# Kernel tuning notes

Hardware: AMD Instinct MI355X
Metric: run time of the kernel (lower is better)

Reference implementation:

```python
import jax, jax.numpy as jnp
from jax import lax
import numpy as np

# torch.sign(torch.sign(x) + 0.5): maps x<0 -> -1, x>=0 -> +1 (zeros go to +1)
def binarize(x):
    return jnp.where(x >= 0, 1.0, -1.0).astype(x.dtype)


def setup_inputs() -> dict:
    key = jax.random.key(0)
    kx, kw, kb = jax.random.split(key, 3)
    x = jax.random.normal(kx, (32, 256, 56, 56), dtype=jnp.float32)
    weight = jax.random.normal(kw, (256, 256, 3, 3), dtype=jnp.float32)
    bias = jax.random.normal(kb, (256,), dtype=jnp.float32)
    return {"x": x, "weight": weight, "bias": bias}


def reference(x, weight, bias):
    b_weight = binarize(weight)  # [O, I, kH, kW] in {-1, +1}
    b_bias = binarize(bias)      # [O] in {-1, +1}
    out = lax.conv_general_dilated(
        x, b_weight,
        window_strides=(1, 1),
        padding=((1, 1), (1, 1)),
        rhs_dilation=(1, 1),
        feature_group_count=1,
        dimension_numbers=("NCHW", "OIHW", "NCHW"),
    )
    return out + b_bias[None, :, None, None]
```

## Files before the change

### kernel.cpp

```cpp
#include <hip/hip_runtime.h>
#include <stdint.h>


#define N_IMG 32
#define C_IN  256
#define H_IN  56
#define W_IN  56
#define O_OUT 256
#define HW    (H_IN * W_IN)
#define K_RAW (C_IN * 9)

typedef int8_t i8x16 __attribute__((ext_vector_type(16)));
typedef int    i32x4 __attribute__((ext_vector_type(4)));
typedef float  f32x4 __attribute__((ext_vector_type(4)));
typedef __bf16 bf16x8 __attribute__((ext_vector_type(8)));

#define XQ_WSTR (58 * 64)
#define XQ_CSTR (58 * 58 * 64)
#define XQ_BYTES ((size_t)N_IMG * 4 * XQ_CSTR)
#define WQ_BYTES ((size_t)36 * 256 * 64)
#define AM_OFF   (XQ_BYTES + WQ_BYTES)
#define WS_NEED  (AM_OFF + 64)

#define BPITCH  80
#define BS_ROWB (58 * BPITCH)

#define AS1 __attribute__((address_space(1)))
#define AS3 __attribute__((address_space(3)))

__device__ __forceinline__ void dma16(const void* g, void* l) {
    __builtin_amdgcn_global_load_lds((const AS1 uint32_t*)g, (AS3 uint32_t*)l, 16, 0, 0);
}

__global__ void amax_zero(unsigned* am) {
    if (threadIdx.x == 0 && blockIdx.x == 0) *am = 0u;
}

__global__ void amax_kernel(const float* __restrict__ x, unsigned* __restrict__ am) {
    const size_t NV = (size_t)N_IMG * C_IN * HW / 4;
    float m = 0.f;
    for (size_t i = (size_t)blockIdx.x * 256 + threadIdx.x; i < NV;
         i += (size_t)gridDim.x * 256) {
        f32x4 v = ((const f32x4*)x)[i];
        m = fmaxf(m, fmaxf(fmaxf(fabsf(v[0]), fabsf(v[1])),
                           fmaxf(fabsf(v[2]), fabsf(v[3]))));
    }
#pragma unroll
    for (int off = 32; off; off >>= 1)
        m = fmaxf(m, __shfl_down(m, off));
    __shared__ float red[4];
    if ((threadIdx.x & 63) == 0) red[threadIdx.x >> 6] = m;
    __syncthreads();
    if (threadIdx.x == 0) {
        m = fmaxf(fmaxf(red[0], red[1]), fmaxf(red[2], red[3]));
        atomicMax(am, __float_as_uint(m));
    }
}

__global__ void xtrans_q(const float* __restrict__ x, int8_t* __restrict__ xq,
                         const unsigned* __restrict__ amax_bits) {
    const int bx = blockIdx.x;
    const int cc = blockIdx.y;
    const int n  = blockIdx.z;
    const int t  = threadIdx.x;
    int8_t* plane = xq + (size_t)(n * 4 + cc) * XQ_CSTR;

    if (bx >= 56) {
        const int hh = (bx == 56) ? 0 : 57;
        if (t < 232) *(i32x4*)(plane + (size_t)hh * XQ_WSTR + t * 16) = (i32x4){0, 0, 0, 0};
        return;
    }
    const int hh = bx + 1;
    const int wg = t & 15;
    const int cg = t >> 4;
    int8_t* orow = plane + (size_t)hh * XQ_WSTR;

    if (wg >= 14) {
        const int ww = (wg == 14) ? 0 : 57;
        *(int*)(orow + ww * 64 + cg * 4) = 0;
        return;
    }

    const float am    = __uint_as_float(*amax_bits);
    const float scale = 127.f / fmaxf(am, 1e-20f);

    const float* src = x + ((size_t)n * C_IN + cc * 64 + cg * 4) * HW
                         + (size_t)bx * W_IN + wg * 4;
    int8_t qb[4][4];
#pragma unroll
    for (int j = 0; j < 4; ++j) {
        f32x4 v = *(const f32x4*)(src + (size_t)j * HW);
#pragma unroll
        for (int k = 0; k < 4; ++k) {
            float f = v[k] * scale;
            f = fminf(fmaxf(f, -127.f), 127.f);
            qb[j][k] = (int8_t)(int)rintf(f);
        }
    }
#pragma unroll
    for (int k = 0; k < 4; ++k) {
        int d = (int)(uint8_t)qb[0][k] | ((int)(uint8_t)qb[1][k] << 8)
              | ((int)(uint8_t)qb[2][k] << 16) | ((int)(uint8_t)qb[3][k] << 24);
        *(int*)(orow + (wg * 4 + k + 1) * 64 + cg * 4) = d;
    }
}

__global__ void wshuf_q(const float* __restrict__ w, int8_t* __restrict__ wq) {
    int idx  = blockIdx.x * 256 + threadIdx.x;
    int cpos = idx & 3;
    int o    = (idx >> 2) & 255;
    int st   = idx >> 10;
    int tap  = st % 9;
    int cc   = st / 9;
    int truec = (cpos - ((o & 15) >> 1)) & 3;
    i8x16 v;
#pragma unroll
    for (int j = 0; j < 16; ++j) {
        int ch = cc * 64 + truec * 16 + j;
        float f = w[(size_t)o * K_RAW + ch * 9 + tap];
        v[j] = (f >= 0.0f) ? (int8_t)1 : (int8_t)-1;
    }
    *(i8x16*)(wq + (size_t)idx * 16) = v;
}

__launch_bounds__(256, 3)
__global__ void bconv_i8(const int8_t* __restrict__ xq,
                         const int8_t* __restrict__ wq,
                         const float* __restrict__ bias,
                         const unsigned* __restrict__ amax_bits,
                         float* __restrict__ out) {
    __shared__ __attribute__((aligned(16))) int8_t As[2 * 8192];
    __shared__ __attribute__((aligned(16))) int8_t Bs[6 * BS_ROWB];

    const int tid  = threadIdx.x;
    const int lane = tid & 63;
    const int wv   = tid >> 6;
    const int row  = lane & 15;
    const int quad = lane >> 4;

    const int nrp  = blockIdx.x;
    const int n    = nrp / 14;
    const int rp   = nrp - n * 14;
    const int oblk = blockIdx.y;
    const int h0   = rp * 4;

    int pr[4], pc[4];
    bool live[4];
#pragma unroll
    for (int nt = 0; nt < 4; ++nt) {
        int p = wv * 64 + nt * 16 + row;
        live[nt] = (p < 224);
        int r = p / 56;
        int c = p - r * 56;
        if (!live[nt]) { r = 0; c = 0; }
        pr[nt] = r;
        pc[nt] = c;
    }

    i32x4 acc[8][4];
#pragma unroll
    for (int mt = 0; mt < 8; ++mt)
#pragma unroll
        for (int nt = 0; nt < 4; ++nt)
            acc[mt][nt] = (i32x4){0, 0, 0, 0};

    const int rowA = row * 64 + (((quad + (row >> 1)) & 3) << 4);
    int addrB[4];
#pragma unroll
    for (int nt = 0; nt < 4; ++nt)
        addrB[nt] = pr[nt] * BS_ROWB + pc[nt] * BPITCH + quad * 16;

    auto issueA = [&](int s) {
        const int8_t* g = wq + (size_t)s * 16384 + oblk * 8192 + wv * 2048 + lane * 16;
        int8_t* l = &As[(s & 1) * 8192 + wv * 2048];
        dma16(g, l);
        dma16(g + 1024, l + 1024);
    };

    issueA(0);

    i32x4 af[8], bc[4], bn[4];

    for (int cc = 0; cc < 4; ++cc) {
        const int s0 = cc * 9;
        __syncthreads();
        if (tid < 232) {
            const int8_t* bbase = xq + (size_t)(n * 4 + cc) * XQ_CSTR
                                     + (size_t)h0 * XQ_WSTR + tid * 16;
            int8_t* ldst = &Bs[(tid >> 2) * BPITCH + (tid & 3) * 16];
            i32x4 hv[6];
#pragma unroll
            for (int r6 = 0; r6 < 6; ++r6)
                hv[r6] = *(const i32x4*)(bbase + r6 * XQ_WSTR);
#pragma unroll
            for (int r6 = 0; r6 < 6; ++r6)
                *(i32x4*)(ldst + r6 * BS_ROWB) = hv[r6];
        }
        __syncthreads();
        issueA(s0 + 1);

        const int8_t* Acur = &As[(s0 & 1) * 8192];
#pragma unroll
        for (int mt = 0; mt < 8; ++mt)
            af[mt] = *(const i32x4*)(Acur + mt * 1024 + rowA);
#pragma unroll
        for (int nt = 0; nt < 4; ++nt)
            bc[nt] = *(const i32x4*)(&Bs[addrB[nt]]);

#pragma unroll
        for (int tap = 0; tap < 9; ++tap) {
            const int s = s0 + tap;
            if (tap < 8) {
                __syncthreads();
                if (s + 2 < 36) issueA(s + 2);
                const int off2 = ((tap + 1) / 3) * BS_ROWB + ((tap + 1) % 3) * BPITCH;
#pragma unroll
                for (int nt = 0; nt < 4; ++nt)
                    bn[nt] = *(const i32x4*)(&Bs[addrB[nt] + off2]);
                const int8_t* Anext = &As[((s + 1) & 1) * 8192];
#pragma unroll
                for (int mt = 0; mt < 8; ++mt) {
                    i32x4 a = af[mt];
#pragma unroll
                    for (int nt = 0; nt < 4; ++nt)
                        acc[mt][nt] = __builtin_amdgcn_mfma_i32_16x16x64_i8(
                            a, bc[nt], acc[mt][nt], 0, 0, 0);
                    af[mt] = *(const i32x4*)(Anext + mt * 1024 + rowA);
                }
#pragma unroll
                for (int nt = 0; nt < 4; ++nt) bc[nt] = bn[nt];
            } else {
#pragma unroll
                for (int mt = 0; mt < 8; ++mt)
#pragma unroll
                    for (int nt = 0; nt < 4; ++nt)
                        acc[mt][nt] = __builtin_amdgcn_mfma_i32_16x16x64_i8(
                            af[mt], bc[nt], acc[mt][nt], 0, 0, 0);
            }
        }
    }

    const float am  = __uint_as_float(*amax_bits);
    const float inv = am * (1.0f / 127.0f);
#pragma unroll
    for (int nt = 0; nt < 4; ++nt) {
        if (!live[nt]) continue;
        float* obase = out + ((size_t)n * O_OUT + oblk * 128) * HW
                           + (h0 + pr[nt]) * W_IN + pc[nt];
#pragma unroll
        for (int mt = 0; mt < 8; ++mt) {
#pragma unroll
            for (int r = 0; r < 4; ++r) {
                int ol = mt * 16 + quad * 4 + r;
                float sb = (bias[oblk * 128 + ol] >= 0.0f) ? 1.0f : -1.0f;
                obase[(size_t)ol * HW] = (float)acc[mt][nt][r] * inv + sb;
            }
        }
    }
}

#define CHW (C_IN * HW)
#define FPITCH 40

__launch_bounds__(256, 2)
__global__ void bconv_fallback(const float* __restrict__ x,
                               const float* __restrict__ w,
                               const float* __restrict__ bias,
                               float* __restrict__ out) {
    __shared__ __attribute__((aligned(16))) __bf16 Asf[128 * FPITCH];
    __shared__ __attribute__((aligned(16))) __bf16 Bsf[128 * FPITCH];

    const int tid  = threadIdx.x;
    const int lane = tid & 63;
    const int wv   = tid >> 6;
    const int pblk = blockIdx.x;
    const int oblk = blockIdx.y;

    const int p_local = tid & 127;
    const int cgrp    = tid >> 7;
    const int pixel   = pblk * 128 + p_local;
    const int n_img   = pixel / HW;
    const int hw      = pixel - n_img * HW;
    const int h       = hw / W_IN;
    const int wx      = hw - h * W_IN;
    const float* xbase = x + (size_t)n_img * CHW;

    f32x4 acc[8][2];
#pragma unroll
    for (int mt = 0; mt < 8; ++mt)
#pragma unroll
        for (int nt = 0; nt < 2; ++nt)
            acc[mt][nt] = (f32x4){0.f, 0.f, 0.f, 0.f};

    const int pix_wave = wv * 32;
    const int row  = lane & 15;
    const int quad = lane >> 4;

    for (int tap = 0; tap < 9; ++tap) {
        const int dh = tap / 3 - 1;
        const int dw = tap % 3 - 1;
        const int hh = h + dh;
        const int ww = wx + dw;
        const bool valid = ((unsigned)hh < (unsigned)H_IN) && ((unsigned)ww < (unsigned)W_IN);
        const int offs = hh * W_IN + ww;

        for (int ck = 0; ck < 8; ++ck) {
            __syncthreads();
#pragma unroll
            for (int rep = 0; rep < 2; ++rep) {
                int v  = tid + rep * 256;
                int oa = v >> 2;
                int c8 = v & 3;
                const float* wsrc = w + (size_t)(oblk * 128 + oa) * K_RAW
                                      + (ck * 32 + c8 * 8) * 9 + tap;
                bf16x8 val;
#pragma unroll
                for (int j = 0; j < 8; ++j)
                    val[j] = (wsrc[j * 9] >= 0.0f) ? (__bf16)1.0f : (__bf16)(-1.0f);
                *(bf16x8*)(&Asf[oa * FPITCH + c8 * 8]) = val;
            }
            {
                const int cbase = (ck * 32 + cgrp * 16) * HW + offs;
#pragma unroll
                for (int g = 0; g < 2; ++g) {
                    bf16x8 vb;
#pragma unroll
                    for (int j = 0; j < 8; ++j) {
                        float f = valid ? xbase[cbase + (g * 8 + j) * HW] : 0.0f;
                        vb[j] = (__bf16)f;
                    }
                    *(bf16x8*)(&Bsf[p_local * FPITCH + cgrp * 16 + g * 8]) = vb;
                }
            }
            __syncthreads();
            bf16x8 bfrag[2];
#pragma unroll
            for (int nt = 0; nt < 2; ++nt)
                bfrag[nt] = *(const bf16x8*)(&Bsf[(pix_wave + nt * 16 + row) * FPITCH + quad * 8]);
#pragma unroll
            for (int mt = 0; mt < 8; ++mt) {
                bf16x8 afrag = *(const bf16x8*)(&Asf[(mt * 16 + row) * FPITCH + quad * 8]);
#pragma unroll
                for (int nt = 0; nt < 2; ++nt)
                    acc[mt][nt] = __builtin_amdgcn_mfma_f32_16x16x32_bf16(
                        afrag, bfrag[nt], acc[mt][nt], 0, 0, 0);
            }
        }
    }

#pragma unroll
    for (int nt = 0; nt < 2; ++nt) {
        int pix = pblk * 128 + pix_wave + nt * 16 + row;
        int ni  = pix / HW;
        int phw = pix - ni * HW;
        float* obase = out + (size_t)ni * (O_OUT * HW) + phw;
#pragma unroll
        for (int mt = 0; mt < 8; ++mt) {
            int o0 = oblk * 128 + mt * 16 + quad * 4;
#pragma unroll
            for (int r = 0; r < 4; ++r) {
                int o = o0 + r;
                float sb = (bias[o] >= 0.0f) ? 1.0f : -1.0f;
                obase[(size_t)o * HW] = acc[mt][nt][r] + sb;
            }
        }
    }
}

extern "C" void kernel_launch(void* const* d_in, const int* in_sizes, int n_in,
                              void* d_out, int out_size, void* d_ws, size_t ws_size,
                              hipStream_t stream) {
    const float* x    = (const float*)d_in[0];
    const float* w    = (const float*)d_in[1];
    const float* bias = (const float*)d_in[2];
    float* out        = (float*)d_out;

    if (ws_size >= WS_NEED) {
        int8_t*   xq = (int8_t*)d_ws;
        int8_t*   wq = (int8_t*)d_ws + XQ_BYTES;
        unsigned* am = (unsigned*)((char*)d_ws + AM_OFF);

        amax_zero<<<1, 64, 0, stream>>>(am);
        amax_kernel<<<1024, 256, 0, stream>>>(x, am);
        xtrans_q<<<dim3(58, 4, N_IMG), dim3(256), 0, stream>>>(x, xq, am);
        wshuf_q<<<144, 256, 0, stream>>>(w, wq);
        bconv_i8<<<dim3(N_IMG * 14, 2), dim3(256), 0, stream>>>(xq, wq, bias, am, out);
    } else {
        bconv_fallback<<<dim3((N_IMG * HW) / 128, 2), dim3(256), 0, stream>>>(
            x, w, bias, out);
    }
}
```

Measured before the change: 331.2 us.

## Merge prep kernels, chunk weight DMA per kh-row, vectorize epilogue bias

Merges the amax reduction and weight binarize/shuffle into one launch, writing per-block maxima to an array so the atomic and the zeroing kernel are no longer needed. The quantize kernel then reduces that array itself. The weight shuffle now stages coalesced reads through LDS. In the conv kernel, A tiles are double-buffered in chunks of three taps, so there are fewer barriers per channel chunk; this triples the A LDS footprint and lowers the occupancy hint from 3 to 2. The epilogue also loads bias as vectors and reorders the stores.

Result: faster. 271.6 us (-18.0%).

```diff
diff --git a/kernel.cpp b/kernel.cpp
--- a/kernel.cpp
+++ b/kernel.cpp
@@ -13,6 +13,7 @@
 typedef int8_t i8x16 __attribute__((ext_vector_type(16)));
 typedef int    i32x4 __attribute__((ext_vector_type(4)));
 typedef float  f32x4 __attribute__((ext_vector_type(4)));
+typedef float  f32x4u __attribute__((ext_vector_type(4), aligned(4)));
 typedef __bf16 bf16x8 __attribute__((ext_vector_type(8)));
 
 #define XQ_WSTR (58 * 64)
@@ -20,10 +21,14 @@
 #define XQ_BYTES ((size_t)N_IMG * 4 * XQ_CSTR)
 #define WQ_BYTES ((size_t)36 * 256 * 64)
 #define AM_OFF   (XQ_BYTES + WQ_BYTES)
-#define WS_NEED  (AM_OFF + 64)
+#define ARR_OFF  (AM_OFF + 64)
+#define WS_NEED  (ARR_OFF + 4096)
 
 #define BPITCH  80
 #define BS_ROWB (58 * BPITCH)
+#define CHUNK_B (3 * 8192)
+
+#define AMAX_BLOCKS 1024
 
 #define AS1 __attribute__((address_space(1)))
 #define AS3 __attribute__((address_space(3)))
@@ -32,39 +37,90 @@
     __builtin_amdgcn_global_load_lds((const AS1 uint32_t*)g, (AS3 uint32_t*)l, 16, 0, 0);
 }
 
-__global__ void amax_zero(unsigned* am) {
-    if (threadIdx.x == 0 && blockIdx.x == 0) *am = 0u;
-}
-
-__global__ void amax_kernel(const float* __restrict__ x, unsigned* __restrict__ am) {
-    const size_t NV = (size_t)N_IMG * C_IN * HW / 4;
-    float m = 0.f;
-    for (size_t i = (size_t)blockIdx.x * 256 + threadIdx.x; i < NV;
-         i += (size_t)gridDim.x * 256) {
-        f32x4 v = ((const f32x4*)x)[i];
-        m = fmaxf(m, fmaxf(fmaxf(fabsf(v[0]), fabsf(v[1])),
-                           fmaxf(fabsf(v[2]), fabsf(v[3]))));
-    }
+__global__ void prep_combo(const float* __restrict__ x, const float* __restrict__ w,
+                           int8_t* __restrict__ wq, float* __restrict__ am_arr) {
+    __shared__ __attribute__((aligned(16))) int8_t S[9 * 64 * 64];
+    const int bx = blockIdx.x;
+    const int t  = threadIdx.x;
+
+    if (bx >= 16) {
+        const int b = bx - 16;
+        const size_t NV = (size_t)N_IMG * C_IN * HW / 4;
+        float m = 0.f;
+        for (size_t i = (size_t)b * 256 + t; i < NV; i += (size_t)AMAX_BLOCKS * 256) {
+            f32x4 v = ((const f32x4*)x)[i];
+            m = fmaxf(m, fmaxf(fmaxf(fabsf(v[0]), fabsf(v[1])),
+                               fmaxf(fabsf(v[2]), fabsf(v[3]))));
+        }
+#pragma unroll
+        for (int off = 32; off; off >>= 1)
+            m = fmaxf(m, __shfl_down(m, off));
+        float* red = (float*)S;
+        if ((t & 63) == 0) red[t >> 6] = m;
+        __syncthreads();
+        if (t == 0)
+            am_arr[b] = fmaxf(fmaxf(red[0], red[1]), fmaxf(red[2], red[3]));
+        return;
+    }
+
+    const int og = bx >> 2;
+    const int cc = bx & 3;
+    const int o0 = og * 64;
+#pragma unroll
+    for (int kk = 0; kk < 4; ++kk) {
+        const int p   = kk * 256 + t;
+        const int o_l = p >> 4;
+        const int chg = p & 15;
+        const float* src = w + (size_t)(o0 + o_l) * K_RAW + (size_t)(cc * 64 + chg * 4) * 9;
+        f32x4u v[9];
+#pragma unroll
+        for (int q = 0; q < 9; ++q) v[q] = *(const f32x4u*)(src + q * 4);
+#pragma unroll
+        for (int tap = 0; tap < 9; ++tap) {
+            unsigned dw = 0;
+#pragma unroll
+            for (int co = 0; co < 4; ++co) {
+                const int flat = co * 9 + tap;
+                const float fv = v[flat >> 2][flat & 3];
+                dw |= (unsigned)((fv >= 0.f) ? 0x01u : 0xffu) << (co * 8);
+            }
+            *(unsigned*)&S[tap * 4096 + o_l * 64 + chg * 4] = dw;
+        }
+    }
+    __syncthreads();
+#pragma unroll
+    for (int kk = 0; kk < 9; ++kk) {
+        const int c    = kk * 256 + t;
+        const int tap  = c >> 8;
+        const int rem  = c & 255;
+        const int o_l  = rem >> 2;
+        const int cpos = rem & 3;
+        const int truec = (cpos - ((o_l & 15) >> 1)) & 3;
+        i32x4 vv = *(const i32x4*)&S[tap * 4096 + o_l * 64 + truec * 16];
+        *(i32x4*)(wq + ((size_t)(cc * 9 + tap) * 256 + (o0 + o_l)) * 64 + cpos * 16) = vv;
+    }
+}
+
+__global__ void xtrans_q(const float* __restrict__ x, int8_t* __restrict__ xq,
+                         const float* __restrict__ am_arr,
+                         unsigned* __restrict__ am_bits) {
+    __shared__ float red[4];
+    const int t = threadIdx.x;
+    float m = fmaxf(fmaxf(am_arr[t], am_arr[t + 256]),
+                    fmaxf(am_arr[t + 512], am_arr[t + 768]));
 #pragma unroll
     for (int off = 32; off; off >>= 1)
         m = fmaxf(m, __shfl_down(m, off));
-    __shared__ float red[4];
-    if ((threadIdx.x & 63) == 0) red[threadIdx.x >> 6] = m;
+    if ((t & 63) == 0) red[t >> 6] = m;
     __syncthreads();
-    if (threadIdx.x == 0) {
-        m = fmaxf(fmaxf(red[0], red[1]), fmaxf(red[2], red[3]));
-        atomicMax(am, __float_as_uint(m));
-    }
-}
-
-__global__ void xtrans_q(const float* __restrict__ x, int8_t* __restrict__ xq,
-                         const unsigned* __restrict__ amax_bits) {
+    m = fmaxf(fmaxf(red[0], red[1]), fmaxf(red[2], red[3]));
+
     const int bx = blockIdx.x;
     const int cc = blockIdx.y;
     const int n  = blockIdx.z;
-    const int t  = threadIdx.x;
+    if (bx == 0 && cc == 0 && n == 0 && t == 0) *am_bits = __float_as_uint(m);
+
     int8_t* plane = xq + (size_t)(n * 4 + cc) * XQ_CSTR;
-
     if (bx >= 56) {
         const int hh = (bx == 56) ? 0 : 57;
         if (t < 232) *(i32x4*)(plane + (size_t)hh * XQ_WSTR + t * 16) = (i32x4){0, 0, 0, 0};
@@ -81,9 +137,7 @@
         return;
     }
 
-    const float am    = __uint_as_float(*amax_bits);
-    const float scale = 127.f / fmaxf(am, 1e-20f);
-
+    const float scale = 127.f / fmaxf(m, 1e-20f);
     const float* src = x + ((size_t)n * C_IN + cc * 64 + cg * 4) * HW
                          + (size_t)bx * W_IN + wg * 4;
     int8_t qb[4][4];
@@ -105,31 +159,13 @@
     }
 }
 
-__global__ void wshuf_q(const float* __restrict__ w, int8_t* __restrict__ wq) {
-    int idx  = blockIdx.x * 256 + threadIdx.x;
-    int cpos = idx & 3;
-    int o    = (idx >> 2) & 255;
-    int st   = idx >> 10;
-    int tap  = st % 9;
-    int cc   = st / 9;
-    int truec = (cpos - ((o & 15) >> 1)) & 3;
-    i8x16 v;
-#pragma unroll
-    for (int j = 0; j < 16; ++j) {
-        int ch = cc * 64 + truec * 16 + j;
-        float f = w[(size_t)o * K_RAW + ch * 9 + tap];
-        v[j] = (f >= 0.0f) ? (int8_t)1 : (int8_t)-1;
-    }
-    *(i8x16*)(wq + (size_t)idx * 16) = v;
-}
-
-__launch_bounds__(256, 3)
+__launch_bounds__(256, 2)
 __global__ void bconv_i8(const int8_t* __restrict__ xq,
                          const int8_t* __restrict__ wq,
                          const float* __restrict__ bias,
                          const unsigned* __restrict__ amax_bits,
                          float* __restrict__ out) {
-    __shared__ __attribute__((aligned(16))) int8_t As[2 * 8192];
+    __shared__ __attribute__((aligned(16))) int8_t As[2 * CHUNK_B];
     __shared__ __attribute__((aligned(16))) int8_t Bs[6 * BS_ROWB];
 
     const int tid  = threadIdx.x;
@@ -170,19 +206,21 @@
     for (int nt = 0; nt < 4; ++nt)
         addrB[nt] = pr[nt] * BS_ROWB + pc[nt] * BPITCH + quad * 16;
 
-    auto issueA = [&](int s) {
-        const int8_t* g = wq + (size_t)s * 16384 + oblk * 8192 + wv * 2048 + lane * 16;
-        int8_t* l = &As[(s & 1) * 8192 + wv * 2048];
-        dma16(g, l);
-        dma16(g + 1024, l + 1024);
+    auto issueA3 = [&](int c) {
+        const int8_t* g = wq + (size_t)(3 * c) * 16384 + oblk * 8192 + wv * 2048 + lane * 16;
+        int8_t* l = &As[(c & 1) * CHUNK_B + wv * 2048];
+#pragma unroll
+        for (int u = 0; u < 3; ++u) {
+            dma16(g + u * 16384,        l + u * 8192);
+            dma16(g + u * 16384 + 1024, l + u * 8192 + 1024);
+        }
     };
 
-    issueA(0);
+    issueA3(0);
 
     i32x4 af[8], bc[4], bn[4];
 
     for (int cc = 0; cc < 4; ++cc) {
-        const int s0 = cc * 9;
         __syncthreads();
         if (tid < 232) {
             const int8_t* bbase = xq + (size_t)(n * 4 + cc) * XQ_CSTR
@@ -197,64 +235,80 @@
                 *(i32x4*)(ldst + r6 * BS_ROWB) = hv[r6];
         }
         __syncthreads();
-        issueA(s0 + 1);
-
-        const int8_t* Acur = &As[(s0 & 1) * 8192];
-#pragma unroll
-        for (int mt = 0; mt < 8; ++mt)
-            af[mt] = *(const i32x4*)(Acur + mt * 1024 + rowA);
-#pragma unroll
-        for (int nt = 0; nt < 4; ++nt)
-            bc[nt] = *(const i32x4*)(&Bs[addrB[nt]]);
-
-#pragma unroll
-        for (int tap = 0; tap < 9; ++tap) {
-            const int s = s0 + tap;
-            if (tap < 8) {
+
+#pragma unroll
+        for (int k = 0; k < 3; ++k) {
+            const int c = cc * 3 + k;
+            if (k == 0) {
+                if (c + 1 < 12) issueA3(c + 1);
+#pragma unroll
+                for (int nt = 0; nt < 4; ++nt)
+                    bc[nt] = *(const i32x4*)(&Bs[addrB[nt]]);
+            } else {
                 __syncthreads();
-                if (s + 2 < 36) issueA(s + 2);
-                const int off2 = ((tap + 1) / 3) * BS_ROWB + ((tap + 1) % 3) * BPITCH;
-#pragma unroll
-                for (int nt = 0; nt < 4; ++nt)
-                    bn[nt] = *(const i32x4*)(&Bs[addrB[nt] + off2]);
-                const int8_t* Anext = &As[((s + 1) & 1) * 8192];
-#pragma unroll
-                for (int mt = 0; mt < 8; ++mt) {
-                    i32x4 a = af[mt];
+                if (c + 1 < 12) issueA3(c + 1);
+#pragma unroll
+                for (int nt = 0; nt < 4; ++nt) bc[nt] = bn[nt];
+            }
+            const int8_t* Acur = &As[(c & 1) * CHUNK_B];
+#pragma unroll
+            for (int mt = 0; mt < 8; ++mt)
+                af[mt] = *(const i32x4*)(Acur + mt * 1024 + rowA);
+
+#pragma unroll
+            for (int u = 0; u < 3; ++u) {
+                if (u < 2) {
+                    const int offn = k * BS_ROWB + (u + 1) * BPITCH;
 #pragma unroll
                     for (int nt = 0; nt < 4; ++nt)
-                        acc[mt][nt] = __builtin_amdgcn_mfma_i32_16x16x64_i8(
-                            a, bc[nt], acc[mt][nt], 0, 0, 0);
-                    af[mt] = *(const i32x4*)(Anext + mt * 1024 + rowA);
+                        bn[nt] = *(const i32x4*)(&Bs[addrB[nt] + offn]);
+                    const int8_t* Anx = Acur + (u + 1) * 8192;
+#pragma unroll
+                    for (int mt = 0; mt < 8; ++mt) {
+                        i32x4 a = af[mt];
+#pragma unroll
+                        for (int nt = 0; nt < 4; ++nt)
+                            acc[mt][nt] = __builtin_amdgcn_mfma_i32_16x16x64_i8(
+                                a, bc[nt], acc[mt][nt], 0, 0, 0);
+                        af[mt] = *(const i32x4*)(Anx + mt * 1024 + rowA);
+                    }
+#pragma unroll
+                    for (int nt = 0; nt < 4; ++nt) bc[nt] = bn[nt];
+                } else {
+                    if (k < 2) {
+                        const int offn = (k + 1) * BS_ROWB;
+#pragma unroll
+                        for (int nt = 0; nt < 4; ++nt)
+                            bn[nt] = *(const i32x4*)(&Bs[addrB[nt] + offn]);
+                    }
+#pragma unroll
+                    for (int mt = 0; mt < 8; ++mt)
+#pragma unroll
+                        for (int nt = 0; nt < 4; ++nt)
+                            acc[mt][nt] = __builtin_amdgcn_mfma_i32_16x16x64_i8(
+                                af[mt], bc[nt], acc[mt][nt], 0, 0, 0);
                 }
-#pragma unroll
-                for (int nt = 0; nt < 4; ++nt) bc[nt] = bn[nt];
-            } else {
-#pragma unroll
-                for (int mt = 0; mt < 8; ++mt)
-#pragma unroll
-                    for (int nt = 0; nt < 4; ++nt)
-                        acc[mt][nt] = __builtin_amdgcn_mfma_i32_16x16x64_i8(
-                            af[mt], bc[nt], acc[mt][nt], 0, 0, 0);
             }
         }
     }
 
     const float am  = __uint_as_float(*amax_bits);
     const float inv = am * (1.0f / 127.0f);
-#pragma unroll
-    for (int nt = 0; nt < 4; ++nt) {
-        if (!live[nt]) continue;
-        float* obase = out + ((size_t)n * O_OUT + oblk * 128) * HW
-                           + (h0 + pr[nt]) * W_IN + pc[nt];
-#pragma unroll
-        for (int mt = 0; mt < 8; ++mt) {
-#pragma unroll
-            for (int r = 0; r < 4; ++r) {
-                int ol = mt * 16 + quad * 4 + r;
-                float sb = (bias[oblk * 128 + ol] >= 0.0f) ? 1.0f : -1.0f;
-                obase[(size_t)ol * HW] = (float)acc[mt][nt][r] * inv + sb;
-            }
+    float* base0 = out + ((size_t)n * O_OUT + oblk * 128) * HW;
+    int pixoff[4];
+#pragma unroll
+    for (int nt = 0; nt < 4; ++nt)
+        pixoff[nt] = (h0 + pr[nt]) * W_IN + pc[nt];
+#pragma unroll
+    for (int mt = 0; mt < 8; ++mt) {
+        f32x4 bv = *(const f32x4*)(bias + oblk * 128 + mt * 16 + quad * 4);
+#pragma unroll
+        for (int r = 0; r < 4; ++r) {
+            const float sb = (bv[r] >= 0.0f) ? 1.0f : -1.0f;
+            const size_t ob = (size_t)(mt * 16 + quad * 4 + r) * HW;
+#pragma unroll
+            for (int nt = 0; nt < 4; ++nt)
+                if (live[nt]) base0[ob + pixoff[nt]] = (float)acc[mt][nt][r] * inv + sb;
         }
     }
 }
@@ -376,14 +430,13 @@
     float* out        = (float*)d_out;
 
     if (ws_size >= WS_NEED) {
-        int8_t*   xq = (int8_t*)d_ws;
-        int8_t*   wq = (int8_t*)d_ws + XQ_BYTES;
-        unsigned* am = (unsigned*)((char*)d_ws + AM_OFF);
-
-        amax_zero<<<1, 64, 0, stream>>>(am);
-        amax_kernel<<<1024, 256, 0, stream>>>(x, am);
-        xtrans_q<<<dim3(58, 4, N_IMG), dim3(256), 0, stream>>>(x, xq, am);
-        wshuf_q<<<144, 256, 0, stream>>>(w, wq);
+        int8_t*   xq     = (int8_t*)d_ws;
+        int8_t*   wq     = (int8_t*)d_ws + XQ_BYTES;
+        unsigned* am     = (unsigned*)((char*)d_ws + AM_OFF);
+        float*    am_arr = (float*)((char*)d_ws + ARR_OFF);
+
+        prep_combo<<<dim3(16 + AMAX_BLOCKS), dim3(256), 0, stream>>>(x, w, wq, am_arr);
+        xtrans_q<<<dim3(58, 4, N_IMG), dim3(256), 0, stream>>>(x, xq, am_arr, am);
         bconv_i8<<<dim3(N_IMG * 14, 2), dim3(256), 0, stream>>>(xq, wq, bias, am, out);
     } else {
         bconv_fallback<<<dim3((N_IMG * HW) / 128, 2), dim3(256), 0, stream>>>(
```
